# Optimization experiments

Hardware: AMD Instinct MI355X
Metric: run time of the kernel (lower is better)

The kernel has to match this reference:

```python
import jax, jax.numpy as jnp
import numpy as np

M_BITS = 8   # mantissa bits (m in BlockQuantize)
E_BITS = 8   # exponent bits (e)
GROUP_D = 64 # column-group width from group_shapes [64,64]


def bfp_quantize_2d(W, d=GROUP_D, m=M_BITS, e=E_BITS):
    """Faithful vectorized BlockQuantize2D with calculate_bias=True.
    Groups = 64-wide column blocks spanning all rows (tensor.reshape(-1,d)[start::new_width])."""
    a, b = W.shape
    nw = b // d
    # [nw, a*d]: each row is one quantization group
    blocks = W.reshape(a, nw, d).transpose(1, 0, 2).reshape(nw, a * d)
    maxv = jnp.max(jnp.abs(blocks), axis=1, keepdims=True)
    bias = 2.0 ** e - jnp.log2(maxv) + jnp.log2(2.0 - 2.0 ** (-m + 1)) - 1.0
    max_exp = 2.0 ** e - 1.0 - bias
    max_val = 2.0 ** max_exp * (1.0 + (1.0 - 2.0 ** (-m - 1)))
    sign = jnp.sign(blocks)
    absx = jnp.clip(jnp.abs(blocks), -max_val, max_val)  # lower bound negative -> no-op, as in source
    exponent = jnp.floor(jnp.log2(absx + 1e-40))
    mantissa = absx / 2.0 ** exponent                    # in [1, 2)
    group_exp = jnp.max(exponent, axis=1, keepdims=True)
    group_exp = jnp.where(group_exp + bias < 1.0, -bias, group_exp)
    # shiftTruncateInBinaryForm
    factor = 2 ** (m - 1)                                # 128
    sm = (mantissa * factor).astype(jnp.int32)           # [128, 256)
    shift = jnp.clip((group_exp - exponent).astype(jnp.int32), 0, 31)
    shifted = jnp.right_shift(sm, shift)
    safe = jnp.maximum(shifted, 1)
    bitlen = (jnp.floor(jnp.log2(safe.astype(jnp.float32))) + 1.0).astype(jnp.int32)
    mask = jnp.where(bitlen > 8, jnp.left_shift(jnp.int32(255), bitlen - 8), jnp.int32(255))
    trunc = jnp.bitwise_and(shifted, mask).astype(jnp.float32) / factor
    q = sign * trunc * 2.0 ** group_exp
    return q.reshape(nw, a, d).transpose(1, 0, 2).reshape(a, b)


def apply_rope(t, cos, sin):
    """t: [b,s,h,hd]; complex rotation on (even, odd) pairs as in apply_rotary_emb."""
    tr = t.reshape(*t.shape[:-1], -1, 2)
    te, to = tr[..., 0], tr[..., 1]
    c = cos[None, :, None, :]
    s = sin[None, :, None, :]
    oe = te * c - to * s
    oo = te * s + to * c
    return jnp.stack([oe, oo], axis=-1).reshape(t.shape)


def setup_inputs() -> dict:
    key = jax.random.key(0)
    k = jax.random.split(key, 5)
    dim, n_heads, n_kv, hd = 4096, 32, 8, 128
    b, s = 1, 2048
    x = jax.random.normal(k[0], (b, s, dim), jnp.float32)
    wq = jax.random.normal(k[1], (n_heads * hd, dim), jnp.float32) * 0.02
    wk = jax.random.normal(k[2], (n_kv * hd, dim), jnp.float32) * 0.02
    wv = jax.random.normal(k[3], (n_kv * hd, dim), jnp.float32) * 0.02
    wo = jax.random.normal(k[4], (dim, n_heads * hd), jnp.float32) * 0.02
    inv_freq = 1.0 / (10000.0 ** (jnp.arange(0, hd, 2, dtype=jnp.float32) / hd))
    ang = jnp.outer(jnp.arange(s, dtype=jnp.float32), inv_freq)  # [s, hd/2]
    return {"x": x, "wq": wq, "wk": wk, "wv": wv, "wo": wo,
            "freqs_cos": jnp.cos(ang), "freqs_sin": jnp.sin(ang)}


def reference(x, wq, wk, wv, wo, freqs_cos, freqs_sin):
    b, s, dim = x.shape
    n_heads, n_kv, hd = 32, 8, 128
    n_rep = n_heads // n_kv
    # block-floating-point quantization of projection weights (per-64-column groups)
    wq_q = bfp_quantize_2d(wq)
    wk_q = bfp_quantize_2d(wk)
    wv_q = bfp_quantize_2d(wv)
    wo_q = bfp_quantize_2d(wo)
    q = jnp.einsum('bsd,od->bso', x, wq_q).reshape(b, s, n_heads, hd)
    kk = jnp.einsum('bsd,od->bso', x, wk_q).reshape(b, s, n_kv, hd)
    v = jnp.einsum('bsd,od->bso', x, wv_q).reshape(b, s, n_kv, hd)
    q = apply_rope(q, freqs_cos, freqs_sin)
    kk = apply_rope(kk, freqs_cos, freqs_sin)
    # repeat_kv: GQA expand kv heads by n_rep
    kk = jnp.repeat(kk, n_rep, axis=2)  # [b,s,n_heads,hd]
    v = jnp.repeat(v, n_rep, axis=2)
    scores = jnp.einsum('bshd,bthd->bhst', q, kk) / jnp.sqrt(jnp.float32(hd))
    causal = jnp.triu(jnp.full((s, s), -jnp.inf, dtype=scores.dtype), k=1)
    probs = jax.nn.softmax(scores + causal, axis=-1)
    out = jnp.einsum('bhst,bthd->bshd', probs, v).reshape(b, s, n_heads * hd)
    return jnp.einsum('bso,do->bsd', out, wo_q)
```

## Files before the change

### kernel.cpp

```cpp
#include <hip/hip_runtime.h>
#include <hip/hip_bf16.h>

typedef __hip_bfloat16 hbf16;
typedef __bf16 bf16x8 __attribute__((ext_vector_type(8)));
typedef float f32x4 __attribute__((ext_vector_type(4)));

#define MFMA16(a, b, c) __builtin_amdgcn_mfma_f32_16x16x32_bf16((a), (b), (c), 0, 0, 0)

#define ASYNC16(ldsaddr, gaddr)                                                        \
  __builtin_amdgcn_global_load_lds(                                                    \
      (__attribute__((address_space(1))) void*)(void*)(gaddr),                         \
      (__attribute__((address_space(3))) void*)(ldsaddr), 16, 0, 0)

static __device__ __forceinline__ float fexp2(float x) {
#if __has_builtin(__builtin_amdgcn_exp2f)
  return __builtin_amdgcn_exp2f(x);
#else
  return exp2f(x);
#endif
}

__global__ void quant_max_kernel(const float* __restrict__ wq, const float* __restrict__ wk,
                                 const float* __restrict__ wv, const float* __restrict__ wo,
                                 unsigned int* __restrict__ gmaxs) {
  const int my = blockIdx.y;
  const float* W;
  int slotBase, rowsPerSplit;
  if (my == 0) { W = wq; slotBase = 0;   rowsPerSplit = 512; }
  else if (my == 1) { W = wk; slotBase = 64;  rowsPerSplit = 128; }
  else if (my == 2) { W = wv; slotBase = 128; rowsPerSplit = 128; }
  else { W = wo; slotBase = 192; rowsPerSplit = 512; }
  const int tid = threadIdx.x;
  const int group = blockIdx.x & 63;
  const int split = blockIdx.x >> 6;
  const int c4 = (tid & 15) * 4;
  const int rs = tid >> 4;
  const float* base = W + (size_t)(split * rowsPerSplit) * 4096 + group * 64 + c4;
  float m = 0.f;
  for (int r = rs; r < rowsPerSplit; r += 16) {
    float4 v = *(const float4*)(base + (size_t)r * 4096);
    m = fmaxf(m, fmaxf(fmaxf(fabsf(v.x), fabsf(v.y)), fmaxf(fabsf(v.z), fabsf(v.w))));
  }
  for (int d = 1; d < 64; d <<= 1) m = fmaxf(m, __shfl_xor(m, d, 64));
  __shared__ float wm_[4];
  if ((tid & 63) == 0) wm_[tid >> 6] = m;
  __syncthreads();
  if (tid == 0) {
    m = fmaxf(fmaxf(wm_[0], wm_[1]), fmaxf(wm_[2], wm_[3]));
    gmaxs[(slotBase + group) * 8 + split] = __float_as_uint(m);
  }
}

__device__ __forceinline__ void quant_body(const float* __restrict__ W, hbf16* __restrict__ Wq,
                                           const unsigned int* __restrict__ gmaxs, int slotBase,
                                           int n4, int block0, int nblocks) {
  const int stride = nblocks * 256;
  const int idx0 = block0 * 256 + (int)threadIdx.x;
  if (idx0 >= n4) return;
  const int slot = slotBase + ((idx0 & 1023) >> 4);
  unsigned int mb = 0;
#pragma unroll
  for (int sp = 0; sp < 8; ++sp) mb = max(mb, gmaxs[slot * 8 + sp]);
  int gex = (int)((mb >> 23) & 255) - 127;
  float s = __uint_as_float((unsigned)(134 - gex) << 23);
  float inv = __uint_as_float((unsigned)(120 + gex) << 23);
  for (int idx = idx0; idx < n4; idx += stride) {
    float4 w = *(const float4*)(W + (size_t)idx * 4);
    hbf16 t[4];
    t[0] = __float2bfloat16(truncf(w.x * s) * inv);
    t[1] = __float2bfloat16(truncf(w.y * s) * inv);
    t[2] = __float2bfloat16(truncf(w.z * s) * inv);
    t[3] = __float2bfloat16(truncf(w.w * s) * inv);
    *(uint2*)(Wq + (size_t)idx * 4) = *(uint2*)t;
  }
}

__global__ void prep_kernel(const float* __restrict__ wq, const float* __restrict__ wk,
                            const float* __restrict__ wv, const float* __restrict__ x,
                            hbf16* __restrict__ Wqkv, hbf16* __restrict__ xb,
                            const unsigned int* __restrict__ gmaxs) {
  const int my = blockIdx.y;
  if (my == 0) {
    quant_body(wq, Wqkv, gmaxs, 0, 4096 * 4096 / 4, blockIdx.x, gridDim.x);
  } else if (my == 1) {
    quant_body(wk, Wqkv + (size_t)4096 * 4096, gmaxs, 64, 1024 * 4096 / 4, blockIdx.x, gridDim.x);
  } else if (my == 2) {
    quant_body(wv, Wqkv + (size_t)5120 * 4096, gmaxs, 128, 1024 * 4096 / 4, blockIdx.x, gridDim.x);
  } else {
    const int stride = gridDim.x * 256;
    for (int idx = blockIdx.x * 256 + threadIdx.x; idx < 2048 * 4096 / 4; idx += stride) {
      float4 v = *(const float4*)(x + (size_t)idx * 4);
      hbf16 t[4] = {__float2bfloat16(v.x), __float2bfloat16(v.y),
                    __float2bfloat16(v.z), __float2bfloat16(v.w)};
      *(uint2*)(xb + (size_t)idx * 4) = *(uint2*)t;
    }
  }
}

__global__ void postproc_kernel(const float* __restrict__ wo, hbf16* __restrict__ woq,
                                const unsigned int* __restrict__ gmaxs,
                                const float* __restrict__ qkv, const float* __restrict__ Cs,
                                const float* __restrict__ Sn, hbf16* __restrict__ qrope,
                                hbf16* __restrict__ krope, hbf16* __restrict__ Vt, float qscale) {
  __shared__ float tile[64][65];
  const int bid = blockIdx.x;
  const int tid = threadIdx.x;
  if (bid < 2048) {
    quant_body(wo, woq, gmaxs, 192, 4096 * 4096 / 4, bid, 2048);
  } else if (bid < 18432) {
    int i = (bid - 2048) * 256 + tid;
    int s = i >> 11, p = i & 2047, t = p & 63;
    float2 q = *(const float2*)(qkv + (size_t)s * 6144 + p * 2);
    float c = Cs[s * 64 + t] * qscale, sn = Sn[s * 64 + t] * qscale;
    hbf16 o[2] = {__float2bfloat16(q.x * c - q.y * sn), __float2bfloat16(q.x * sn + q.y * c)};
    *(unsigned int*)(qrope + (size_t)s * 4096 + p * 2) = *(unsigned int*)o;
  } else if (bid < 22528) {
    int i = (bid - 18432) * 256 + tid;
    int s = i >> 9, p = i & 511, t = p & 63;
    float2 q = *(const float2*)(qkv + (size_t)s * 6144 + 4096 + p * 2);
    float c = Cs[s * 64 + t], sn = Sn[s * 64 + t];
    hbf16 o[2] = {__float2bfloat16(q.x * c - q.y * sn), __float2bfloat16(q.x * sn + q.y * c)};
    *(unsigned int*)(krope + (size_t)s * 1024 + p * 2) = *(unsigned int*)o;
  } else {
    int id = bid - 22528;
    int g = id & 7, sb = (id >> 3) & 31, db = id >> 8;
    int c = tid & 63;
    for (int r = tid >> 6; r < 64; r += 4)
      tile[r][c] = qkv[(size_t)(sb * 64 + r) * 6144 + 5120 + g * 128 + db * 64 + c];
    __syncthreads();
    for (int r = tid >> 6; r < 64; r += 4)
      Vt[(size_t)g * 262144 + (size_t)(db * 64 + r) * 2048 + sb * 64 + c] =
          __float2bfloat16(tile[c][r]);
  }
}

__global__ __launch_bounds__(512, 2) void gemm8_kernel(const hbf16* __restrict__ A,
                                                       const hbf16* __restrict__ Bt,
                                                       float* __restrict__ C, int N) {
  constexpr int K = 4096;
  constexpr int NT = K / 64;
  constexpr int TILE = 128 * 128 + 256 * 128;
  __shared__ __align__(16) char smem[3 * TILE];
  const int tid = threadIdx.x;
  const int wave = tid >> 6, lane = tid & 63;
  const int l15 = lane & 15, quad = lane >> 4;
  const int bm = blockIdx.x, bn = blockIdx.y;
  const int wm = (wave >> 2) * 64, wn = (wave & 3) * 64;

  const char* Ab = (const char*)(A + (size_t)bm * 128 * K);
  const char* Bb = (const char*)(Bt + (size_t)bn * 256 * K);

  f32x4 acc[4][4];
#pragma unroll
  for (int i = 0; i < 4; ++i)
#pragma unroll
    for (int n = 0; n < 4; ++n) acc[i][n] = (f32x4){0.f, 0.f, 0.f, 0.f};

  auto stageA = [&](char* buf, int kk) {
#pragma unroll
    for (int r = 0; r < 2; ++r) {
      int f = r * 8192 + tid * 16;
      int row = f >> 7;
      int lc = ((f >> 4) & 7) ^ (row & 7);
      ASYNC16(buf + f, Ab + (size_t)row * (K * 2) + kk * 2 + lc * 16);
    }
  };
  auto stageB = [&](char* buf, int kk) {
#pragma unroll
    for (int r = 0; r < 4; ++r) {
      int f = r * 8192 + tid * 16;
      int row = f >> 7;
      int lc = ((f >> 4) & 7) ^ (row & 7);
      ASYNC16(buf + 16384 + f, Bb + (size_t)row * (K * 2) + kk * 2 + lc * 16);
    }
  };

  stageA(smem, 0);
  stageB(smem, 0);
  stageA(smem + TILE, 64);
  stageB(smem + TILE, 64);
  asm volatile("s_waitcnt vmcnt(6)" ::: "memory");
  __builtin_amdgcn_s_barrier();

  int cur = 0;
  for (int t = 0; t < NT; ++t) {
    const char* sa = smem + cur * TILE;
    const char* sb = sa + 16384;
    const int nxt2 = (cur >= 1) ? cur - 1 : 2;
    char* stg = smem + nxt2 * TILE;
    const int kk2 = ((t + 2 < NT) ? t + 2 : NT - 1) * 64;

    bf16x8 af[2][4], b0[2][2];
#pragma unroll
    for (int kc = 0; kc < 2; ++kc) {
      const int cx = (((kc << 2) | quad) ^ (l15 & 7)) * 16;
#pragma unroll
      for (int i = 0; i < 4; ++i)
        af[kc][i] = *(const bf16x8*)(sa + (wm + i * 16 + l15) * 128 + cx);
#pragma unroll
      for (int n = 0; n < 2; ++n)
        b0[kc][n] = *(const bf16x8*)(sb + (wn + n * 16 + l15) * 128 + cx);
    }
    stageA(stg, kk2);
    __builtin_amdgcn_s_barrier();
    __builtin_amdgcn_s_setprio(1);
#pragma unroll
    for (int kc = 0; kc < 2; ++kc)
#pragma unroll
      for (int i = 0; i < 4; ++i)
#pragma unroll
        for (int n = 0; n < 2; ++n) acc[i][n] = MFMA16(af[kc][i], b0[kc][n], acc[i][n]);
    __builtin_amdgcn_s_setprio(0);
    __builtin_amdgcn_s_barrier();

    bf16x8 b1[2][2];
#pragma unroll
    for (int kc = 0; kc < 2; ++kc) {
      const int cx = (((kc << 2) | quad) ^ (l15 & 7)) * 16;
#pragma unroll
      for (int n = 0; n < 2; ++n)
        b1[kc][n] = *(const bf16x8*)(sb + (wn + (n + 2) * 16 + l15) * 128 + cx);
    }
    stageB(stg, kk2);
    asm volatile("s_waitcnt vmcnt(6)" ::: "memory");
    __builtin_amdgcn_s_barrier();
    __builtin_amdgcn_s_setprio(1);
#pragma unroll
    for (int kc = 0; kc < 2; ++kc)
#pragma unroll
      for (int i = 0; i < 4; ++i)
#pragma unroll
        for (int n = 0; n < 2; ++n)
          acc[i][n + 2] = MFMA16(af[kc][i], b1[kc][n], acc[i][n + 2]);
    __builtin_amdgcn_s_setprio(0);
    __builtin_amdgcn_s_barrier();

    cur = (cur == 2) ? 0 : cur + 1;
  }

#pragma unroll
  for (int i = 0; i < 4; ++i) {
    int row = bm * 128 + wm + i * 16 + quad * 4;
#pragma unroll
    for (int n = 0; n < 4; ++n) {
      float* cp = C + (size_t)row * N + bn * 256 + wn + n * 16 + l15;
#pragma unroll
      for (int r = 0; r < 4; ++r) cp[(size_t)r * N] = acc[i][n][r];
    }
  }
}

__global__ __launch_bounds__(256, 4) void attn_kernel(const hbf16* __restrict__ Q,
                                                      const hbf16* __restrict__ Kr,
                                                      const hbf16* __restrict__ Vt,
                                                      hbf16* __restrict__ O) {
  __shared__ __align__(16) hbf16 sK[64 * 128];
  __shared__ __align__(16) hbf16 sV[128 * 64];
  const int tid = threadIdx.x;
  const int wave = tid >> 6, lane = tid & 63;
  const int l15 = lane & 15, quad = lane >> 4;
  const int bid = blockIdx.x;
  const int h = bid >> 5;
  const int qb = (31 - (bid & 31) + 8 * ((bid >> 8) & 3)) & 31;
  const int g = h >> 2;
  const int qrow0 = qb * 64 + wave * 16;
  const int qrow = qrow0 + l15;

  bf16x8 qf[4];
  {
    const hbf16* qp = Q + (size_t)qrow * 4096 + h * 128 + quad * 8;
#pragma unroll
    for (int kc = 0; kc < 4; ++kc) qf[kc] = *(const bf16x8*)(qp + kc * 32);
  }
  f32x4 of[8];
#pragma unroll
  for (int nf = 0; nf < 8; ++nf) of[nf] = (f32x4){0.f, 0.f, 0.f, 0.f};
  float m_i = -1e30f, l_i = 0.f;

  const char* Kb = (const char*)Kr + (size_t)g * 256;
  const char* Vb = (const char*)Vt + (size_t)g * 524288;
  char* sKb = (char*)sK;
  char* sVb = (char*)sV;

  const int nkb = qb + 1;
  for (int kb = 0; kb < nkb; ++kb) {
#pragma unroll
    for (int r = 0; r < 4; ++r) {
      int f = r * 4096 + tid * 16;
      {
        int row = f >> 8;
        int lc = ((f >> 4) & 15) ^ (row & 15);
        ASYNC16(sKb + f, Kb + (size_t)(kb * 64 + row) * 2048 + lc * 16);
      }
      {
        int row = f >> 7;
        int lc = ((f >> 4) & 7) ^ (row & 7);
        ASYNC16(sVb + f, Vb + (size_t)row * 4096 + kb * 128 + lc * 16);
      }
    }
    __syncthreads();

    f32x4 sacc[4];
#pragma unroll
    for (int n = 0; n < 4; ++n) sacc[n] = (f32x4){0.f, 0.f, 0.f, 0.f};
#pragma unroll
    for (int n = 0; n < 4; ++n)
#pragma unroll
      for (int kc = 0; kc < 4; ++kc) {
        bf16x8 kf = *(const bf16x8*)(sKb + (n * 16 + l15) * 256 +
                                     (((kc << 2) | quad) ^ l15) * 16);
        sacc[n] = MFMA16(kf, qf[kc], sacc[n]);
      }

    float p[4][4];
    float mx = -1e30f;
    if (kb == qb) {
      const int key0 = kb * 64 + quad * 4;
#pragma unroll
      for (int n = 0; n < 4; ++n)
#pragma unroll
        for (int r = 0; r < 4; ++r) {
          float s = sacc[n][r];
          s = (key0 + n * 16 + r > qrow) ? -1e30f : s;
          p[n][r] = s;
          mx = fmaxf(mx, s);
        }
    } else {
#pragma unroll
      for (int n = 0; n < 4; ++n)
#pragma unroll
        for (int r = 0; r < 4; ++r) {
          p[n][r] = sacc[n][r];
          mx = fmaxf(mx, sacc[n][r]);
        }
    }
    mx = fmaxf(mx, __shfl_xor(mx, 16, 64));
    mx = fmaxf(mx, __shfl_xor(mx, 32, 64));
    float mnew = fmaxf(m_i, mx);
    float alpha = fexp2(m_i - mnew);
    m_i = mnew;
    float sum = 0.f;
#pragma unroll
    for (int n = 0; n < 4; ++n)
#pragma unroll
      for (int r = 0; r < 4; ++r) {
        p[n][r] = fexp2(p[n][r] - mnew);
        sum += p[n][r];
      }
    sum += __shfl_xor(sum, 16, 64);
    sum += __shfl_xor(sum, 32, 64);
    l_i = l_i * alpha + sum;
#pragma unroll
    for (int nf = 0; nf < 8; ++nf)
#pragma unroll
      for (int r = 0; r < 4; ++r) of[nf][r] *= alpha;

    unsigned pk[8];
#pragma unroll
    for (int n = 0; n < 4; ++n)
#pragma unroll
      for (int h2 = 0; h2 < 2; ++h2) {
        hbf16 t2[2] = {__float2bfloat16(p[n][2 * h2]), __float2bfloat16(p[n][2 * h2 + 1])};
        pk[n * 2 + h2] = *(unsigned*)t2;
      }

    const int sa = ((quad & 1) << 5) + l15;
    const int sb2 = sa + 16;
#pragma unroll
    for (int kc = 0; kc < 2; ++kc) {
      unsigned a0 = __shfl((int)pk[kc * 4 + 0], sa, 64);
      unsigned a1 = __shfl((int)pk[kc * 4 + 1], sa, 64);
      unsigned a2 = __shfl((int)pk[kc * 4 + 2], sa, 64);
      unsigned a3 = __shfl((int)pk[kc * 4 + 3], sa, 64);
      unsigned b0 = __shfl((int)pk[kc * 4 + 0], sb2, 64);
      unsigned b1 = __shfl((int)pk[kc * 4 + 1], sb2, 64);
      unsigned b2 = __shfl((int)pk[kc * 4 + 2], sb2, 64);
      unsigned b3 = __shfl((int)pk[kc * 4 + 3], sb2, 64);
      union {
        unsigned u[4];
        bf16x8 v;
      } pf;
      pf.u[0] = (quad < 2) ? a0 : a2;
      pf.u[1] = (quad < 2) ? a1 : a3;
      pf.u[2] = (quad < 2) ? b0 : b2;
      pf.u[3] = (quad < 2) ? b1 : b3;
#pragma unroll
      for (int nf = 0; nf < 8; ++nf) {
        bf16x8 vf = *(const bf16x8*)(sVb + (nf * 16 + l15) * 128 +
                                     (((kc << 2) | quad) ^ (l15 & 7)) * 16);
        of[nf] = MFMA16(vf, pf.v, of[nf]);
      }
    }
    __syncthreads();
  }

  const float invl = 1.f / l_i;
#pragma unroll
  for (int nf = 0; nf < 8; ++nf) {
    hbf16 t4[4];
#pragma unroll
    for (int r = 0; r < 4; ++r) t4[r] = __float2bfloat16(of[nf][r] * invl);
    *(uint2*)(O + (size_t)qrow * 4096 + h * 128 + nf * 16 + quad * 4) = *(uint2*)t4;
  }
}

extern "C" void kernel_launch(void* const* d_in, const int* in_sizes, int n_in,
                              void* d_out, int out_size, void* d_ws, size_t ws_size,
                              hipStream_t stream) {
  const float* x = (const float*)d_in[0];
  const float* wq = (const float*)d_in[1];
  const float* wk = (const float*)d_in[2];
  const float* wv = (const float*)d_in[3];
  const float* wo = (const float*)d_in[4];
  const float* fc = (const float*)d_in[5];
  const float* fs = (const float*)d_in[6];
  float* out = (float*)d_out;

  char* w = (char*)d_ws;
  size_t off = 0;
  auto alloc = [&](size_t bytes) -> char* {
    char* p = w + off;
    off += (bytes + 255) & ~(size_t)255;
    return p;
  };
  unsigned int* gmaxs = (unsigned int*)alloc(256 * 8 * 4);
  hbf16* xb = (hbf16*)alloc((size_t)2048 * 4096 * 2);
  hbf16* wqkv = (hbf16*)alloc((size_t)6144 * 4096 * 2);
  float* qkv = (float*)alloc((size_t)2048 * 6144 * 4);
  hbf16* qrope = (hbf16*)alloc((size_t)2048 * 4096 * 2);
  hbf16* krope = (hbf16*)alloc((size_t)2048 * 1024 * 2);
  hbf16* vt = (hbf16*)alloc((size_t)8 * 128 * 2048 * 2);
  hbf16* woq = wqkv;
  hbf16* attno = (hbf16*)qkv;

  const float kSc = 0.12753139668280277f;

  quant_max_kernel<<<dim3(512, 4), 256, 0, stream>>>(wq, wk, wv, wo, gmaxs);
  prep_kernel<<<dim3(2048, 4), 256, 0, stream>>>(wq, wk, wv, x, wqkv, xb, gmaxs);
  gemm8_kernel<<<dim3(16, 24), 512, 0, stream>>>(xb, wqkv, qkv, 6144);
  postproc_kernel<<<23040, 256, 0, stream>>>(wo, woq, gmaxs, qkv, fc, fs, qrope, krope, vt, kSc);
  attn_kernel<<<1024, 256, 0, stream>>>(qrope, krope, vt, attno);
  gemm8_kernel<<<dim3(16, 16), 512, 0, stream>>>(attno, woq, out, 4096);
  (void)in_sizes; (void)n_in; (void)out_size; (void)ws_size;
}
```

Measured before the change: 555.7 us.

## Use 256x256 GEMM tiles with four-phase pipeline and split-K output projection

The 128x256 triple-buffered GEMM is replaced with a 256x256 tile kernel that uses four half-tile LDS slots per stage, double-buffered (128KB LDS), computed in four quadrant phases. Each wave's accumulator count doubles, giving more reuse per loaded byte. The QKV GEMM drops to 192 blocks. The output projection is split along K into two halves writing separate buffers, then summed by an extra elementwise kernel. This trades fewer, larger tiles and better arithmetic intensity for higher register pressure, under-filled CUs with only 192/256 blocks, and an extra 32MB read-modify-write pass.

```diff
diff --git a/kernel.cpp b/kernel.cpp
--- a/kernel.cpp
+++ b/kernel.cpp
@@ -134,120 +134,167 @@
   }
 }
 
-__global__ __launch_bounds__(512, 2) void gemm8_kernel(const hbf16* __restrict__ A,
-                                                       const hbf16* __restrict__ Bt,
-                                                       float* __restrict__ C, int N) {
-  constexpr int K = 4096;
-  constexpr int NT = K / 64;
-  constexpr int TILE = 128 * 128 + 256 * 128;
-  __shared__ __align__(16) char smem[3 * TILE];
+template <int KLEN>
+__global__ __launch_bounds__(512, 2) void gemm4p_kernel(const hbf16* __restrict__ A,
+                                                        const hbf16* __restrict__ Bt,
+                                                        float* __restrict__ C0,
+                                                        float* __restrict__ C1, int N) {
+  constexpr int LDA = 4096;
+  constexpr int NT = KLEN / 64;
+  __shared__ __align__(16) char smem[131072];
   const int tid = threadIdx.x;
   const int wave = tid >> 6, lane = tid & 63;
   const int l15 = lane & 15, quad = lane >> 4;
-  const int bm = blockIdx.x, bn = blockIdx.y;
-  const int wm = (wave >> 2) * 64, wn = (wave & 3) * 64;
-
-  const char* Ab = (const char*)(A + (size_t)bm * 128 * K);
-  const char* Bb = (const char*)(Bt + (size_t)bn * 256 * K);
-
-  f32x4 acc[4][4];
-#pragma unroll
-  for (int i = 0; i < 4; ++i)
+  const int wm = wave >> 2, wn = wave & 3;
+  const int bm = blockIdx.x, bn = blockIdx.y, bz = blockIdx.z;
+  float* C = bz ? C1 : C0;
+
+  const char* Ab = (const char*)(A + (size_t)bm * 256 * LDA + bz * KLEN);
+  const char* Bb = (const char*)(Bt + (size_t)bn * 256 * LDA + bz * KLEN);
+  char* sm = (char*)smem;
+
+#define SA_(par, mh) (((par)*2 + (mh)) * 16384)
+#define SB_(par, nh) (65536 + ((par)*2 + (nh)) * 16384)
+
+  f32x4 acc[8][4];
+#pragma unroll
+  for (int i = 0; i < 8; ++i)
 #pragma unroll
     for (int n = 0; n < 4; ++n) acc[i][n] = (f32x4){0.f, 0.f, 0.f, 0.f};
 
-  auto stageA = [&](char* buf, int kk) {
+  auto stage = [&](int slotOff, const char* gb, int rowOff, int tu) {
+    const int kk = ((tu < NT) ? tu : NT - 1) * 64;
 #pragma unroll
     for (int r = 0; r < 2; ++r) {
       int f = r * 8192 + tid * 16;
       int row = f >> 7;
       int lc = ((f >> 4) & 7) ^ (row & 7);
-      ASYNC16(buf + f, Ab + (size_t)row * (K * 2) + kk * 2 + lc * 16);
+      ASYNC16(sm + slotOff + f, gb + (size_t)(rowOff + row) * (LDA * 2) + kk * 2 + lc * 16);
     }
   };
-  auto stageB = [&](char* buf, int kk) {
-#pragma unroll
-    for (int r = 0; r < 4; ++r) {
-      int f = r * 8192 + tid * 16;
-      int row = f >> 7;
-      int lc = ((f >> 4) & 7) ^ (row & 7);
-      ASYNC16(buf + 16384 + f, Bb + (size_t)row * (K * 2) + kk * 2 + lc * 16);
-    }
-  };
-
-  stageA(smem, 0);
-  stageB(smem, 0);
-  stageA(smem + TILE, 64);
-  stageB(smem + TILE, 64);
-  asm volatile("s_waitcnt vmcnt(6)" ::: "memory");
+
+  stage(SA_(0, 0), Ab, 0, 0);
+  stage(SB_(0, 0), Bb, 0, 0);
+  stage(SA_(0, 1), Ab, 128, 0);
+  stage(SB_(0, 1), Bb, 128, 0);
+  stage(SA_(1, 0), Ab, 0, 1);
+  stage(SB_(1, 0), Bb, 0, 1);
+  asm volatile("s_waitcnt vmcnt(4)" ::: "memory");
   __builtin_amdgcn_s_barrier();
 
-  int cur = 0;
+  const int aoff = (wm * 16 + l15) * 128;
+  const int boff = (wn * 16 + l15) * 128;
+  const int cx0 = (quad ^ (l15 & 7)) * 16;
+  const int cx1 = ((4 | quad) ^ (l15 & 7)) * 16;
+
   for (int t = 0; t < NT; ++t) {
-    const char* sa = smem + cur * TILE;
-    const char* sb = sa + 16384;
-    const int nxt2 = (cur >= 1) ? cur - 1 : 2;
-    char* stg = smem + nxt2 * TILE;
-    const int kk2 = ((t + 2 < NT) ? t + 2 : NT - 1) * 64;
-
-    bf16x8 af[2][4], b0[2][2];
-#pragma unroll
-    for (int kc = 0; kc < 2; ++kc) {
-      const int cx = (((kc << 2) | quad) ^ (l15 & 7)) * 16;
-#pragma unroll
-      for (int i = 0; i < 4; ++i)
-        af[kc][i] = *(const bf16x8*)(sa + (wm + i * 16 + l15) * 128 + cx);
-#pragma unroll
-      for (int n = 0; n < 2; ++n)
-        b0[kc][n] = *(const bf16x8*)(sb + (wn + n * 16 + l15) * 128 + cx);
-    }
-    stageA(stg, kk2);
+    const int par = t & 1, par1 = par ^ 1;
+    bf16x8 af[2][4], bg[2][2];
+
+#pragma unroll
+    for (int mf = 0; mf < 4; ++mf) {
+      af[0][mf] = *(const bf16x8*)(sm + SA_(par, 0) + aoff + mf * 4096 + cx0);
+      af[1][mf] = *(const bf16x8*)(sm + SA_(par, 0) + aoff + mf * 4096 + cx1);
+    }
+#pragma unroll
+    for (int nf = 0; nf < 2; ++nf) {
+      bg[0][nf] = *(const bf16x8*)(sm + SB_(par, 0) + boff + nf * 8192 + cx0);
+      bg[1][nf] = *(const bf16x8*)(sm + SB_(par, 0) + boff + nf * 8192 + cx1);
+    }
+    stage(SA_(par1, 1), Ab, 128, t + 1);
     __builtin_amdgcn_s_barrier();
     __builtin_amdgcn_s_setprio(1);
 #pragma unroll
     for (int kc = 0; kc < 2; ++kc)
 #pragma unroll
-      for (int i = 0; i < 4; ++i)
-#pragma unroll
-        for (int n = 0; n < 2; ++n) acc[i][n] = MFMA16(af[kc][i], b0[kc][n], acc[i][n]);
+      for (int mf = 0; mf < 4; ++mf)
+#pragma unroll
+        for (int nf = 0; nf < 2; ++nf) acc[mf][nf] = MFMA16(af[kc][mf], bg[kc][nf], acc[mf][nf]);
     __builtin_amdgcn_s_setprio(0);
     __builtin_amdgcn_s_barrier();
 
-    bf16x8 b1[2][2];
-#pragma unroll
-    for (int kc = 0; kc < 2; ++kc) {
-      const int cx = (((kc << 2) | quad) ^ (l15 & 7)) * 16;
-#pragma unroll
-      for (int n = 0; n < 2; ++n)
-        b1[kc][n] = *(const bf16x8*)(sb + (wn + (n + 2) * 16 + l15) * 128 + cx);
-    }
-    stageB(stg, kk2);
-    asm volatile("s_waitcnt vmcnt(6)" ::: "memory");
+#pragma unroll
+    for (int nf = 0; nf < 2; ++nf) {
+      bg[0][nf] = *(const bf16x8*)(sm + SB_(par, 1) + boff + nf * 8192 + cx0);
+      bg[1][nf] = *(const bf16x8*)(sm + SB_(par, 1) + boff + nf * 8192 + cx1);
+    }
+    stage(SB_(par1, 1), Bb, 128, t + 1);
     __builtin_amdgcn_s_barrier();
     __builtin_amdgcn_s_setprio(1);
 #pragma unroll
     for (int kc = 0; kc < 2; ++kc)
 #pragma unroll
-      for (int i = 0; i < 4; ++i)
-#pragma unroll
-        for (int n = 0; n < 2; ++n)
-          acc[i][n + 2] = MFMA16(af[kc][i], b1[kc][n], acc[i][n + 2]);
+      for (int mf = 0; mf < 4; ++mf)
+#pragma unroll
+        for (int nf = 0; nf < 2; ++nf)
+          acc[mf][nf + 2] = MFMA16(af[kc][mf], bg[kc][nf], acc[mf][nf + 2]);
     __builtin_amdgcn_s_setprio(0);
     __builtin_amdgcn_s_barrier();
 
-    cur = (cur == 2) ? 0 : cur + 1;
-  }
-
-#pragma unroll
-  for (int i = 0; i < 4; ++i) {
-    int row = bm * 128 + wm + i * 16 + quad * 4;
+#pragma unroll
+    for (int mf = 0; mf < 4; ++mf) {
+      af[0][mf] = *(const bf16x8*)(sm + SA_(par, 1) + aoff + mf * 4096 + cx0);
+      af[1][mf] = *(const bf16x8*)(sm + SA_(par, 1) + aoff + mf * 4096 + cx1);
+    }
+#pragma unroll
+    for (int nf = 0; nf < 2; ++nf) {
+      bg[0][nf] = *(const bf16x8*)(sm + SB_(par, 0) + boff + nf * 8192 + cx0);
+      bg[1][nf] = *(const bf16x8*)(sm + SB_(par, 0) + boff + nf * 8192 + cx1);
+    }
+    stage(SA_(par, 0), Ab, 0, t + 2);
+    __builtin_amdgcn_s_barrier();
+    __builtin_amdgcn_s_setprio(1);
+#pragma unroll
+    for (int kc = 0; kc < 2; ++kc)
+#pragma unroll
+      for (int mf = 0; mf < 4; ++mf)
+#pragma unroll
+        for (int nf = 0; nf < 2; ++nf)
+          acc[mf + 4][nf] = MFMA16(af[kc][mf], bg[kc][nf], acc[mf + 4][nf]);
+    __builtin_amdgcn_s_setprio(0);
+    __builtin_amdgcn_s_barrier();
+
+#pragma unroll
+    for (int nf = 0; nf < 2; ++nf) {
+      bg[0][nf] = *(const bf16x8*)(sm + SB_(par, 1) + boff + nf * 8192 + cx0);
+      bg[1][nf] = *(const bf16x8*)(sm + SB_(par, 1) + boff + nf * 8192 + cx1);
+    }
+    stage(SB_(par, 0), Bb, 0, t + 2);
+    __builtin_amdgcn_s_barrier();
+    __builtin_amdgcn_s_setprio(1);
+#pragma unroll
+    for (int kc = 0; kc < 2; ++kc)
+#pragma unroll
+      for (int mf = 0; mf < 4; ++mf)
+#pragma unroll
+        for (int nf = 0; nf < 2; ++nf)
+          acc[mf + 4][nf + 2] = MFMA16(af[kc][mf], bg[kc][nf], acc[mf + 4][nf + 2]);
+    __builtin_amdgcn_s_setprio(0);
+    asm volatile("s_waitcnt vmcnt(4)" ::: "memory");
+    __builtin_amdgcn_s_barrier();
+  }
+  asm volatile("s_waitcnt vmcnt(0)" ::: "memory");
+
+#pragma unroll
+  for (int j = 0; j < 8; ++j) {
+    const int row = bm * 256 + wm * 16 + j * 32 + quad * 4;
 #pragma unroll
     for (int n = 0; n < 4; ++n) {
-      float* cp = C + (size_t)row * N + bn * 256 + wn + n * 16 + l15;
-#pragma unroll
-      for (int r = 0; r < 4; ++r) cp[(size_t)r * N] = acc[i][n][r];
-    }
-  }
+      float* cp = C + (size_t)row * N + bn * 256 + wn * 16 + n * 64 + l15;
+#pragma unroll
+      for (int r = 0; r < 4; ++r) cp[(size_t)r * N] = acc[j][n][r];
+    }
+  }
+#undef SA_
+#undef SB_
+}
+
+__global__ void addf4_kernel(float* __restrict__ o, const float* __restrict__ a) {
+  const int i = blockIdx.x * 256 + threadIdx.x;
+  float4 x = ((const float4*)o)[i];
+  float4 y = ((const float4*)a)[i];
+  x.x += y.x; x.y += y.y; x.z += y.z; x.w += y.w;
+  ((float4*)o)[i] = x;
 }
 
 __global__ __launch_bounds__(256, 4) void attn_kernel(const hbf16* __restrict__ Q,
@@ -432,14 +479,16 @@
   hbf16* vt = (hbf16*)alloc((size_t)8 * 128 * 2048 * 2);
   hbf16* woq = wqkv;
   hbf16* attno = (hbf16*)qkv;
+  float* c1 = (float*)((char*)qkv + (size_t)2048 * 4096 * 2);
 
   const float kSc = 0.12753139668280277f;
 
   quant_max_kernel<<<dim3(512, 4), 256, 0, stream>>>(wq, wk, wv, wo, gmaxs);
   prep_kernel<<<dim3(2048, 4), 256, 0, stream>>>(wq, wk, wv, x, wqkv, xb, gmaxs);
-  gemm8_kernel<<<dim3(16, 24), 512, 0, stream>>>(xb, wqkv, qkv, 6144);
+  gemm4p_kernel<4096><<<dim3(8, 24), 512, 0, stream>>>(xb, wqkv, qkv, qkv, 6144);
   postproc_kernel<<<23040, 256, 0, stream>>>(wo, woq, gmaxs, qkv, fc, fs, qrope, krope, vt, kSc);
   attn_kernel<<<1024, 256, 0, stream>>>(qrope, krope, vt, attno);
-  gemm8_kernel<<<dim3(16, 16), 512, 0, stream>>>(attno, woq, out, 4096);
+  gemm4p_kernel<2048><<<dim3(8, 16, 2), 512, 0, stream>>>(attno, woq, out, c1, 4096);
+  addf4_kernel<<<8192, 256, 0, stream>>>(out, c1);
   (void)in_sizes; (void)n_in; (void)out_size; (void)ws_size;
 }
```

After: 549.0 us. Within noise of the previous version (-1.2%).

## Restructure GEMM into quarter-tile ping-pong schedule with templated N-tile width

Applied to the files above, without the earlier changes.

Replaces the triple-buffered GEMM with a templated kernel that splits each A and B tile into two halves and double-buffers them. Each k-step runs four MFMA phases, each overlapped with an async load of one half-tile. The QKV projection now uses 384-wide N tiles, giving a 16x16 grid instead of 16x24, so the launch fits in a single wave of blocks. The cost is more barriers per k-step, a larger per-block LDS footprint and a larger accumulator array when NFRAG=6, which could limit occupancy.

```diff
diff --git a/kernel.cpp b/kernel.cpp
--- a/kernel.cpp
+++ b/kernel.cpp
@@ -134,120 +134,160 @@
   }
 }
 
-__global__ __launch_bounds__(512, 2) void gemm8_kernel(const hbf16* __restrict__ A,
-                                                       const hbf16* __restrict__ Bt,
-                                                       float* __restrict__ C, int N) {
+template <int NFRAG>
+__global__ __launch_bounds__(512, 2) void gemm_tp_kernel(const hbf16* __restrict__ A,
+                                                         const hbf16* __restrict__ Bt,
+                                                         float* __restrict__ C, int N) {
   constexpr int K = 4096;
   constexpr int NT = K / 64;
-  constexpr int TILE = 128 * 128 + 256 * 128;
-  __shared__ __align__(16) char smem[3 * TILE];
+  constexpr int HB = NFRAG / 2;
+  constexpr int SBSZ = NFRAG * 4096;
+  constexpr int VM = 1 + HB;
+  __shared__ __align__(16) char smem[32768 + 4 * SBSZ];
   const int tid = threadIdx.x;
   const int wave = tid >> 6, lane = tid & 63;
   const int l15 = lane & 15, quad = lane >> 4;
+  const int wm = wave >> 2, wn = wave & 3;
   const int bm = blockIdx.x, bn = blockIdx.y;
-  const int wm = (wave >> 2) * 64, wn = (wave & 3) * 64;
 
   const char* Ab = (const char*)(A + (size_t)bm * 128 * K);
-  const char* Bb = (const char*)(Bt + (size_t)bn * 256 * K);
-
-  f32x4 acc[4][4];
+  const char* Bb = (const char*)(Bt + (size_t)bn * (NFRAG * 64) * K);
+  char* sm = (char*)smem;
+
+#define SA_(par, mh) (((par)*2 + (mh)) * 8192)
+#define SB_(par, nh) (32768 + ((par)*2 + (nh)) * SBSZ)
+
+  f32x4 acc[4][NFRAG];
 #pragma unroll
   for (int i = 0; i < 4; ++i)
 #pragma unroll
-    for (int n = 0; n < 4; ++n) acc[i][n] = (f32x4){0.f, 0.f, 0.f, 0.f};
-
-  auto stageA = [&](char* buf, int kk) {
-#pragma unroll
-    for (int r = 0; r < 2; ++r) {
+    for (int n = 0; n < NFRAG; ++n) acc[i][n] = (f32x4){0.f, 0.f, 0.f, 0.f};
+
+  auto stageA = [&](int slotOff, int rowOff, int tu) {
+    const int kk = ((tu < NT) ? tu : NT - 1) * 64;
+    int f = tid * 16;
+    int row = f >> 7;
+    int lc = ((f >> 4) & 7) ^ (row & 7);
+    ASYNC16(sm + slotOff + f, Ab + (size_t)(rowOff + row) * (K * 2) + kk * 2 + lc * 16);
+  };
+  auto stageB = [&](int slotOff, int rowOff, int tu) {
+    const int kk = ((tu < NT) ? tu : NT - 1) * 64;
+#pragma unroll
+    for (int r = 0; r < HB; ++r) {
       int f = r * 8192 + tid * 16;
       int row = f >> 7;
       int lc = ((f >> 4) & 7) ^ (row & 7);
-      ASYNC16(buf + f, Ab + (size_t)row * (K * 2) + kk * 2 + lc * 16);
+      ASYNC16(sm + slotOff + f, Bb + (size_t)(rowOff + row) * (K * 2) + kk * 2 + lc * 16);
     }
   };
-  auto stageB = [&](char* buf, int kk) {
-#pragma unroll
-    for (int r = 0; r < 4; ++r) {
-      int f = r * 8192 + tid * 16;
-      int row = f >> 7;
-      int lc = ((f >> 4) & 7) ^ (row & 7);
-      ASYNC16(buf + 16384 + f, Bb + (size_t)row * (K * 2) + kk * 2 + lc * 16);
-    }
-  };
-
-  stageA(smem, 0);
-  stageB(smem, 0);
-  stageA(smem + TILE, 64);
-  stageB(smem + TILE, 64);
-  asm volatile("s_waitcnt vmcnt(6)" ::: "memory");
+
+  stageA(SA_(0, 0), 0, 0);
+  stageB(SB_(0, 0), 0, 0);
+  stageA(SA_(0, 1), 64, 0);
+  stageB(SB_(0, 1), NFRAG * 32, 0);
+  stageA(SA_(1, 0), 0, 1);
+  stageB(SB_(1, 0), 0, 1);
+  asm volatile("s_waitcnt vmcnt(%0)" ::"i"(VM) : "memory");
   __builtin_amdgcn_s_barrier();
 
-  int cur = 0;
+  const int cx0 = (quad ^ (l15 & 7)) * 16;
+  const int cx1 = ((4 | quad) ^ (l15 & 7)) * 16;
+
   for (int t = 0; t < NT; ++t) {
-    const char* sa = smem + cur * TILE;
-    const char* sb = sa + 16384;
-    const int nxt2 = (cur >= 1) ? cur - 1 : 2;
-    char* stg = smem + nxt2 * TILE;
-    const int kk2 = ((t + 2 < NT) ? t + 2 : NT - 1) * 64;
-
-    bf16x8 af[2][4], b0[2][2];
-#pragma unroll
-    for (int kc = 0; kc < 2; ++kc) {
-      const int cx = (((kc << 2) | quad) ^ (l15 & 7)) * 16;
-#pragma unroll
-      for (int i = 0; i < 4; ++i)
-        af[kc][i] = *(const bf16x8*)(sa + (wm + i * 16 + l15) * 128 + cx);
-#pragma unroll
-      for (int n = 0; n < 2; ++n)
-        b0[kc][n] = *(const bf16x8*)(sb + (wn + n * 16 + l15) * 128 + cx);
-    }
-    stageA(stg, kk2);
+    const int par = t & 1, par1 = par ^ 1;
+    bf16x8 af[2][2], bg0[2][HB], bg1[2][HB];
+
+#pragma unroll
+    for (int jl = 0; jl < 2; ++jl) {
+      const int ro = (wm * 16 + jl * 32 + l15) * 128;
+      af[0][jl] = *(const bf16x8*)(sm + SA_(par, 0) + ro + cx0);
+      af[1][jl] = *(const bf16x8*)(sm + SA_(par, 0) + ro + cx1);
+    }
+#pragma unroll
+    for (int nl = 0; nl < HB; ++nl) {
+      const int ro = (wn * 16 + nl * 64 + l15) * 128;
+      bg0[0][nl] = *(const bf16x8*)(sm + SB_(par, 0) + ro + cx0);
+      bg0[1][nl] = *(const bf16x8*)(sm + SB_(par, 0) + ro + cx1);
+    }
+    stageA(SA_(par1, 1), 64, t + 1);
     __builtin_amdgcn_s_barrier();
     __builtin_amdgcn_s_setprio(1);
 #pragma unroll
     for (int kc = 0; kc < 2; ++kc)
 #pragma unroll
-      for (int i = 0; i < 4; ++i)
-#pragma unroll
-        for (int n = 0; n < 2; ++n) acc[i][n] = MFMA16(af[kc][i], b0[kc][n], acc[i][n]);
+      for (int jl = 0; jl < 2; ++jl)
+#pragma unroll
+        for (int nl = 0; nl < HB; ++nl)
+          acc[jl][nl] = MFMA16(af[kc][jl], bg0[kc][nl], acc[jl][nl]);
     __builtin_amdgcn_s_setprio(0);
     __builtin_amdgcn_s_barrier();
 
-    bf16x8 b1[2][2];
-#pragma unroll
-    for (int kc = 0; kc < 2; ++kc) {
-      const int cx = (((kc << 2) | quad) ^ (l15 & 7)) * 16;
-#pragma unroll
-      for (int n = 0; n < 2; ++n)
-        b1[kc][n] = *(const bf16x8*)(sb + (wn + (n + 2) * 16 + l15) * 128 + cx);
-    }
-    stageB(stg, kk2);
-    asm volatile("s_waitcnt vmcnt(6)" ::: "memory");
+#pragma unroll
+    for (int nl = 0; nl < HB; ++nl) {
+      const int ro = (wn * 16 + nl * 64 + l15) * 128;
+      bg1[0][nl] = *(const bf16x8*)(sm + SB_(par, 1) + ro + cx0);
+      bg1[1][nl] = *(const bf16x8*)(sm + SB_(par, 1) + ro + cx1);
+    }
+    stageB(SB_(par1, 1), NFRAG * 32, t + 1);
     __builtin_amdgcn_s_barrier();
     __builtin_amdgcn_s_setprio(1);
 #pragma unroll
     for (int kc = 0; kc < 2; ++kc)
 #pragma unroll
-      for (int i = 0; i < 4; ++i)
-#pragma unroll
-        for (int n = 0; n < 2; ++n)
-          acc[i][n + 2] = MFMA16(af[kc][i], b1[kc][n], acc[i][n + 2]);
+      for (int jl = 0; jl < 2; ++jl)
+#pragma unroll
+        for (int nl = 0; nl < HB; ++nl)
+          acc[jl][HB + nl] = MFMA16(af[kc][jl], bg1[kc][nl], acc[jl][HB + nl]);
     __builtin_amdgcn_s_setprio(0);
     __builtin_amdgcn_s_barrier();
 
-    cur = (cur == 2) ? 0 : cur + 1;
-  }
-
-#pragma unroll
-  for (int i = 0; i < 4; ++i) {
-    int row = bm * 128 + wm + i * 16 + quad * 4;
-#pragma unroll
-    for (int n = 0; n < 4; ++n) {
-      float* cp = C + (size_t)row * N + bn * 256 + wn + n * 16 + l15;
-#pragma unroll
-      for (int r = 0; r < 4; ++r) cp[(size_t)r * N] = acc[i][n][r];
-    }
-  }
+#pragma unroll
+    for (int jl = 0; jl < 2; ++jl) {
+      const int ro = (wm * 16 + jl * 32 + l15) * 128;
+      af[0][jl] = *(const bf16x8*)(sm + SA_(par, 1) + ro + cx0);
+      af[1][jl] = *(const bf16x8*)(sm + SA_(par, 1) + ro + cx1);
+    }
+    stageA(SA_(par, 0), 0, t + 2);
+    __builtin_amdgcn_s_barrier();
+    __builtin_amdgcn_s_setprio(1);
+#pragma unroll
+    for (int kc = 0; kc < 2; ++kc)
+#pragma unroll
+      for (int jl = 0; jl < 2; ++jl)
+#pragma unroll
+        for (int nl = 0; nl < HB; ++nl)
+          acc[2 + jl][nl] = MFMA16(af[kc][jl], bg0[kc][nl], acc[2 + jl][nl]);
+    __builtin_amdgcn_s_setprio(0);
+    __builtin_amdgcn_s_barrier();
+
+    stageB(SB_(par, 0), 0, t + 2);
+    __builtin_amdgcn_s_barrier();
+    __builtin_amdgcn_s_setprio(1);
+#pragma unroll
+    for (int kc = 0; kc < 2; ++kc)
+#pragma unroll
+      for (int jl = 0; jl < 2; ++jl)
+#pragma unroll
+        for (int nl = 0; nl < HB; ++nl)
+          acc[2 + jl][HB + nl] = MFMA16(af[kc][jl], bg1[kc][nl], acc[2 + jl][HB + nl]);
+    __builtin_amdgcn_s_setprio(0);
+    asm volatile("s_waitcnt vmcnt(%0)" ::"i"(VM) : "memory");
+    __builtin_amdgcn_s_barrier();
+  }
+  asm volatile("s_waitcnt vmcnt(0)" ::: "memory");
+
+#pragma unroll
+  for (int j = 0; j < 4; ++j) {
+    const int row = bm * 128 + wm * 16 + j * 32 + quad * 4;
+#pragma unroll
+    for (int n = 0; n < NFRAG; ++n) {
+      float* cp = C + (size_t)row * N + bn * (NFRAG * 64) + wn * 16 + n * 64 + l15;
+#pragma unroll
+      for (int r = 0; r < 4; ++r) cp[(size_t)r * N] = acc[j][n][r];
+    }
+  }
+#undef SA_
+#undef SB_
 }
 
 __global__ __launch_bounds__(256, 4) void attn_kernel(const hbf16* __restrict__ Q,
@@ -437,9 +477,9 @@
 
   quant_max_kernel<<<dim3(512, 4), 256, 0, stream>>>(wq, wk, wv, wo, gmaxs);
   prep_kernel<<<dim3(2048, 4), 256, 0, stream>>>(wq, wk, wv, x, wqkv, xb, gmaxs);
-  gemm8_kernel<<<dim3(16, 24), 512, 0, stream>>>(xb, wqkv, qkv, 6144);
+  gemm_tp_kernel<6><<<dim3(16, 16), 512, 0, stream>>>(xb, wqkv, qkv, 6144);
   postproc_kernel<<<23040, 256, 0, stream>>>(wo, woq, gmaxs, qkv, fc, fs, qrope, krope, vt, kSc);
   attn_kernel<<<1024, 256, 0, stream>>>(qrope, krope, vt, attno);
-  gemm8_kernel<<<dim3(16, 16), 512, 0, stream>>>(attno, woq, out, 4096);
+  gemm_tp_kernel<4><<<dim3(16, 16), 512, 0, stream>>>(attno, woq, out, 4096);
   (void)in_sizes; (void)n_in; (void)out_size; (void)ws_size;
 }
```

Result: faster. 511.6 us (-7.9%).
